# Kernel tuning notes

Measured on AMD Instinct MI355X. Metric: run time of the kernel, lower is better.

Reference implementation:

```python
import jax, jax.numpy as jnp
import numpy as np


def log_g(x):
    # log of the 'continuous' g: g(x) = x + 0.5 for x>=0, sigmoid(x) otherwise
    return jnp.where(x >= 0, jnp.log(jax.nn.relu(x) + 0.5), -jax.nn.softplus(-x))


def setup_inputs() -> dict:
    key = jax.random.key(0)
    ks = jax.random.split(key, 6)
    B, T, D, H = 8, 4096, 1024, 1024
    s = 1.0 / np.sqrt(D)
    return {
        "x": jax.random.normal(ks[0], (B, T, D), dtype=jnp.float32),
        "h_0": jax.random.uniform(ks[1], (B, 1, H), dtype=jnp.float32),
        "Wz": jax.random.normal(ks[2], (D, H), dtype=jnp.float32) * s,
        "bz": jnp.zeros((H,), dtype=jnp.float32),
        "Wh": jax.random.normal(ks[3], (D, H), dtype=jnp.float32) * s,
        "bh": jnp.zeros((H,), dtype=jnp.float32),
    }


def reference(x, h_0, Wz, bz, Wh, bh):
    # x: [B,T,D], h_0: [B,1,H]
    k = jnp.einsum('btd,dh->bth', x, Wz) + bz            # gate pre-activation
    log_z = -jax.nn.softplus(-k)                          # log sigmoid(k)
    log_coeffs = -jax.nn.softplus(k)                      # log (1 - sigmoid(k))
    log_h0 = log_g(h_0)                                   # [B,1,H]
    log_tilde_h = log_g(jnp.einsum('btd,dh->bth', x, Wh) + bh)
    # parallel scan in log space over time axis
    a_star = jnp.pad(jnp.cumsum(log_coeffs, axis=1), ((0, 0), (1, 0), (0, 0)))  # [B,T+1,H]
    log_values = jnp.concatenate([log_h0, log_z + log_tilde_h], axis=1)          # [B,T+1,H]
    log_h = a_star + jax.lax.cumlogsumexp(log_values - a_star, axis=1)
    return jnp.exp(log_h)  # [B,T+1,H]
```

## Files before the change

kernel.cpp:

```cpp
#include <hip/hip_runtime.h>
#include <hip/hip_bf16.h>
#include <cstdint>
#include <cstddef>

#define B_ 8
#define T_ 4096
#define D_ 1024
#define H_ 1024
#define M_ (B_*T_)
#define NCHUNK 64
#define CLEN 64

using bf16x8   = __attribute__((ext_vector_type(8))) __bf16;
using floatx4  = __attribute__((ext_vector_type(4))) float;
using float4v  = __attribute__((ext_vector_type(4))) float;
using ushort4v = __attribute__((ext_vector_type(4))) unsigned short;
using aw2_t    = __attribute__((ext_vector_type(2))) _Float16;
using halfx8   = __attribute__((ext_vector_type(8))) _Float16;

__device__ inline unsigned short f2bf(float f) {
  union { float f; unsigned u; } v; v.f = f;
  unsigned u = v.u;
  u += 0x7fffu + ((u >> 16) & 1u);
  return (unsigned short)(u >> 16);
}

__device__ inline void async_load16(const void* g, void* l) {
  __builtin_amdgcn_global_load_lds((const __attribute__((address_space(1))) void*)g,
                                   (__attribute__((address_space(3))) void*)l,
                                   16, 0, 0);
}

__global__ __launch_bounds__(256) void cast_x_kernel(const float* __restrict__ x,
                                                     unsigned short* __restrict__ xb) {
  size_t i = ((size_t)blockIdx.x * 256 + threadIdx.x) * 2;
#pragma unroll
  for (int j = 0; j < 2; ++j) {
    float4v v = ((const float4v*)x)[i + j];
    ushort4v o = { f2bf(v[0]), f2bf(v[1]), f2bf(v[2]), f2bf(v[3]) };
    ((ushort4v*)xb)[i + j] = o;
  }
}

__global__ __launch_bounds__(256) void transpose_w_kernel(const float* __restrict__ Wz,
                                                          const float* __restrict__ Wh,
                                                          unsigned short* __restrict__ Wzt,
                                                          unsigned short* __restrict__ Wht) {
  __shared__ float tile[32][33];
  const float* W = blockIdx.z ? Wh : Wz;
  unsigned short* Wt = blockIdx.z ? Wht : Wzt;
  int n0 = blockIdx.x * 32, k0 = blockIdx.y * 32;
#pragma unroll
  for (int j = 0; j < 4; ++j) {
    int kr = threadIdx.y + j * 8;
    tile[kr][threadIdx.x] = W[(size_t)(k0 + kr) * H_ + n0 + threadIdx.x];
  }
  __syncthreads();
#pragma unroll
  for (int j = 0; j < 4; ++j) {
    int nr = threadIdx.y + j * 8;
    Wt[(size_t)(n0 + nr) * D_ + k0 + threadIdx.x] = f2bf(tile[threadIdx.x][nr]);
  }
}

__global__ __launch_bounds__(256, 2) void gemm_kernel(
    const unsigned short* __restrict__ xb,
    const unsigned short* __restrict__ wzt,
    const unsigned short* __restrict__ wht,
    const float* __restrict__ bz, const float* __restrict__ bh,
    aw2_t* __restrict__ aw_out) {
  __shared__ __align__(16) unsigned short ldsA[128 * 32];
  __shared__ __align__(16) unsigned short ldsBz[128 * 32];
  __shared__ __align__(16) unsigned short ldsBh[128 * 32];

  const int tid = threadIdx.x;
  const int lane = tid & 63, wid = tid >> 6;
  const int wm = wid >> 1, wn = wid & 1;
  const int row16 = lane & 15, quad = lane >> 4;

  int g = blockIdx.x;
  int x = g & 7, j = g >> 3;
  int n_idx = j & 7;
  int m_idx = (x << 5) | (j >> 3);
  const int m0 = m_idx * 128, n0 = n_idx * 128;

  floatx4 accz[4][4], acch[4][4];
#pragma unroll
  for (int mi = 0; mi < 4; ++mi)
#pragma unroll
    for (int ni = 0; ni < 4; ++ni) {
      accz[mi][ni] = (floatx4){0.f, 0.f, 0.f, 0.f};
      acch[mi][ni] = (floatx4){0.f, 0.f, 0.f, 0.f};
    }

  const unsigned short* a0 = xb  + (size_t)(m0 + (tid >> 2)) * D_ + (tid & 3) * 8;
  const unsigned short* a1 = xb  + (size_t)(m0 + 64 + (tid >> 2)) * D_ + (tid & 3) * 8;
  const unsigned short* z0 = wzt + (size_t)(n0 + (tid >> 2)) * D_ + (tid & 3) * 8;
  const unsigned short* z1 = wzt + (size_t)(n0 + 64 + (tid >> 2)) * D_ + (tid & 3) * 8;
  const unsigned short* h0p = wht + (size_t)(n0 + (tid >> 2)) * D_ + (tid & 3) * 8;
  const unsigned short* h1p = wht + (size_t)(n0 + 64 + (tid >> 2)) * D_ + (tid & 3) * 8;

  for (int kk = 0; kk < D_; kk += 32) {
    async_load16(a0 + kk, &ldsA[tid * 8]);
    async_load16(a1 + kk, &ldsA[(tid + 256) * 8]);
    async_load16(z0 + kk, &ldsBz[tid * 8]);
    async_load16(z1 + kk, &ldsBz[(tid + 256) * 8]);
    async_load16(h0p + kk, &ldsBh[tid * 8]);
    async_load16(h1p + kk, &ldsBh[(tid + 256) * 8]);
    __syncthreads();

    bf16x8 af[4], bzf[4], bhf[4];
#pragma unroll
    for (int mi = 0; mi < 4; ++mi)
      af[mi] = *(const bf16x8*)&ldsA[(wm * 64 + mi * 16 + row16) * 32 + quad * 8];
#pragma unroll
    for (int ni = 0; ni < 4; ++ni) {
      bzf[ni] = *(const bf16x8*)&ldsBz[(wn * 64 + ni * 16 + row16) * 32 + quad * 8];
      bhf[ni] = *(const bf16x8*)&ldsBh[(wn * 64 + ni * 16 + row16) * 32 + quad * 8];
    }
#pragma unroll
    for (int mi = 0; mi < 4; ++mi)
#pragma unroll
      for (int ni = 0; ni < 4; ++ni) {
        accz[mi][ni] = __builtin_amdgcn_mfma_f32_16x16x32_bf16(af[mi], bzf[ni], accz[mi][ni], 0, 0, 0);
        acch[mi][ni] = __builtin_amdgcn_mfma_f32_16x16x32_bf16(af[mi], bhf[ni], acch[mi][ni], 0, 0, 0);
      }
    __syncthreads();
  }

#pragma unroll
  for (int mi = 0; mi < 4; ++mi) {
#pragma unroll
    for (int ni = 0; ni < 4; ++ni) {
      int col = n0 + wn * 64 + ni * 16 + row16;
      float bzv = bz[col], bhv = bh[col];
#pragma unroll
      for (int r = 0; r < 4; ++r) {
        int row = m0 + wm * 64 + mi * 16 + quad * 4 + r;
        float k   = accz[mi][ni][r] + bzv;
        float pre = acch[mi][ni][r] + bhv;
        float z  = 1.f / (1.f + __expf(-k));
        float av = 1.f / (1.f + __expf(k));
        float gg = (pre >= 0.f) ? (pre + 0.5f) : 1.f / (1.f + __expf(-pre));
        aw2_t o = { (_Float16)av, (_Float16)(z * gg) };
        aw_out[(size_t)row * H_ + col] = o;
      }
    }
  }
}

__global__ __launch_bounds__(256) void scan_pass1(const halfx8* __restrict__ aw,
                                                  float* __restrict__ P, float* __restrict__ S) {
  int c = blockIdx.x;
  int b = blockIdx.y;
  int h4 = threadIdx.x;
  size_t base = (size_t)(b * T_ + c * CLEN) * (H_ / 4) + h4;
  float p0 = 1.f, p1 = 1.f, p2 = 1.f, p3 = 1.f;
  float s0 = 0.f, s1 = 0.f, s2 = 0.f, s3 = 0.f;
#pragma unroll 8
  for (int i = 0; i < CLEN; ++i) {
    halfx8 v = aw[base + (size_t)i * (H_ / 4)];
    float a0 = (float)v[0], w0 = (float)v[1];
    float a1 = (float)v[2], w1 = (float)v[3];
    float a2 = (float)v[4], w2 = (float)v[5];
    float a3 = (float)v[6], w3 = (float)v[7];
    s0 = a0 * s0 + w0; p0 *= a0;
    s1 = a1 * s1 + w1; p1 *= a1;
    s2 = a2 * s2 + w2; p2 *= a2;
    s3 = a3 * s3 + w3; p3 *= a3;
  }
  size_t o = ((size_t)b * H_ + h4 * 4) * NCHUNK + c;
  P[o] = p0; P[o + NCHUNK] = p1; P[o + 2 * NCHUNK] = p2; P[o + 3 * NCHUNK] = p3;
  S[o] = s0; S[o + NCHUNK] = s1; S[o + 2 * NCHUNK] = s2; S[o + 3 * NCHUNK] = s3;
}

__global__ __launch_bounds__(256) void scan_pass2(const float* __restrict__ h0,
                                                  const float* __restrict__ P,
                                                  const float* __restrict__ S,
                                                  float* __restrict__ carry,
                                                  float* __restrict__ out) {
  int gid = blockIdx.x * 256 + threadIdx.x;
  int b = gid >> 10, h = gid & 1023;
  float v = h0[(size_t)b * H_ + h];
  float cur = (v >= 0.f) ? (v + 0.5f) : 1.f / (1.f + __expf(-v));
  out[((size_t)b * (T_ + 1)) * H_ + h] = cur;
  const float4v* Pv = (const float4v*)&P[((size_t)b * H_ + h) * NCHUNK];
  const float4v* Sv = (const float4v*)&S[((size_t)b * H_ + h) * NCHUNK];
  float4v* Cv = (float4v*)&carry[((size_t)b * H_ + h) * NCHUNK];
#pragma unroll
  for (int j = 0; j < NCHUNK / 4; ++j) {
    float4v p = Pv[j], s = Sv[j], cc;
    cc[0] = cur; cur = p[0] * cur + s[0];
    cc[1] = cur; cur = p[1] * cur + s[1];
    cc[2] = cur; cur = p[2] * cur + s[2];
    cc[3] = cur; cur = p[3] * cur + s[3];
    Cv[j] = cc;
  }
}

__global__ __launch_bounds__(256) void scan_pass3(const halfx8* __restrict__ aw,
                                                  const float* __restrict__ carry,
                                                  float* __restrict__ out) {
  int c = blockIdx.x;
  int b = blockIdx.y;
  int h4 = threadIdx.x;
  size_t base = (size_t)(b * T_ + c * CLEN) * (H_ / 4) + h4;
  size_t cb = ((size_t)b * H_ + h4 * 4) * NCHUNK + c;
  float c0 = carry[cb], c1 = carry[cb + NCHUNK], c2 = carry[cb + 2 * NCHUNK], c3 = carry[cb + 3 * NCHUNK];
  size_t obase = ((size_t)b * (T_ + 1) + c * CLEN + 1) * (H_ / 4) + h4;
  float4v* outv = (float4v*)out;
#pragma unroll 8
  for (int i = 0; i < CLEN; ++i) {
    halfx8 v = aw[base + (size_t)i * (H_ / 4)];
    c0 = (float)v[0] * c0 + (float)v[1];
    c1 = (float)v[2] * c1 + (float)v[3];
    c2 = (float)v[4] * c2 + (float)v[5];
    c3 = (float)v[6] * c3 + (float)v[7];
    float4v o = { c0, c1, c2, c3 };
    outv[obase + (size_t)i * (H_ / 4)] = o;
  }
}

extern "C" void kernel_launch(void* const* d_in, const int* in_sizes, int n_in,
                              void* d_out, int out_size, void* d_ws, size_t ws_size,
                              hipStream_t stream) {
  const float* x  = (const float*)d_in[0];
  const float* h0 = (const float*)d_in[1];
  const float* Wz = (const float*)d_in[2];
  const float* bz = (const float*)d_in[3];
  const float* Wh = (const float*)d_in[4];
  const float* bh = (const float*)d_in[5];
  float* out = (float*)d_out;

  char* ws = (char*)d_ws;
  unsigned short* xb  = (unsigned short*)(ws);
  unsigned short* wzt = (unsigned short*)(ws + 67108864ULL);
  unsigned short* wht = (unsigned short*)(ws + 69206016ULL);
  aw2_t* aw_ws = (aw2_t*)(ws + 71303168ULL);
  float* P_ws  = (float*)(ws + 71303168ULL + 134217728ULL);
  float* S_ws  = (float*)(ws + 71303168ULL + 134217728ULL + 2097152ULL);
  float* c_ws  = (float*)(ws + 71303168ULL + 134217728ULL + 2ULL * 2097152ULL);

  hipLaunchKernelGGL(cast_x_kernel, dim3(16384), dim3(256), 0, stream, x, xb);
  hipLaunchKernelGGL(transpose_w_kernel, dim3(32, 32, 2), dim3(32, 8), 0, stream, Wz, Wh, wzt, wht);
  hipLaunchKernelGGL(gemm_kernel, dim3(2048), dim3(256), 0, stream,
                     xb, wzt, wht, bz, bh, aw_ws);
  hipLaunchKernelGGL(scan_pass1, dim3(NCHUNK, B_), dim3(256), 0, stream,
                     (const halfx8*)aw_ws, P_ws, S_ws);
  hipLaunchKernelGGL(scan_pass2, dim3(32), dim3(256), 0, stream, h0, P_ws, S_ws, c_ws, out);
  hipLaunchKernelGGL(scan_pass3, dim3(NCHUNK, B_), dim3(256), 0, stream,
                     (const halfx8*)aw_ws, c_ws, out);
}
```

Measured before the change: 493.5 us.

## Double GEMM K-tile to 64 and swizzle LDS layout to avoid bank conflicts

The fused dual GEMM now stages a 64-wide K slice per iteration instead of 32, which halves the number of barrier pairs per tile. It also applies an XOR/rotation swizzle to the 16-byte chunks in LDS so that MFMA fragment reads spread across banks. The cost is doubled LDS use (48KB per block), which may limit occupancy at two blocks per CU.

```diff
diff --git a/kernel.cpp b/kernel.cpp
--- a/kernel.cpp
+++ b/kernel.cpp
@@ -69,9 +69,9 @@
     const unsigned short* __restrict__ wht,
     const float* __restrict__ bz, const float* __restrict__ bh,
     aw2_t* __restrict__ aw_out) {
-  __shared__ __align__(16) unsigned short ldsA[128 * 32];
-  __shared__ __align__(16) unsigned short ldsBz[128 * 32];
-  __shared__ __align__(16) unsigned short ldsBh[128 * 32];
+  __shared__ __align__(16) unsigned short ldsA[128 * 64];
+  __shared__ __align__(16) unsigned short ldsBz[128 * 64];
+  __shared__ __align__(16) unsigned short ldsBh[128 * 64];
 
   const int tid = threadIdx.x;
   const int lane = tid & 63, wid = tid >> 6;
@@ -93,38 +93,46 @@
       acch[mi][ni] = (floatx4){0.f, 0.f, 0.f, 0.f};
     }
 
-  const unsigned short* a0 = xb  + (size_t)(m0 + (tid >> 2)) * D_ + (tid & 3) * 8;
-  const unsigned short* a1 = xb  + (size_t)(m0 + 64 + (tid >> 2)) * D_ + (tid & 3) * 8;
-  const unsigned short* z0 = wzt + (size_t)(n0 + (tid >> 2)) * D_ + (tid & 3) * 8;
-  const unsigned short* z1 = wzt + (size_t)(n0 + 64 + (tid >> 2)) * D_ + (tid & 3) * 8;
-  const unsigned short* h0p = wht + (size_t)(n0 + (tid >> 2)) * D_ + (tid & 3) * 8;
-  const unsigned short* h1p = wht + (size_t)(n0 + 64 + (tid >> 2)) * D_ + (tid & 3) * 8;
-
-  for (int kk = 0; kk < D_; kk += 32) {
-    async_load16(a0 + kk, &ldsA[tid * 8]);
-    async_load16(a1 + kk, &ldsA[(tid + 256) * 8]);
-    async_load16(z0 + kk, &ldsBz[tid * 8]);
-    async_load16(z1 + kk, &ldsBz[(tid + 256) * 8]);
-    async_load16(h0p + kk, &ldsBh[tid * 8]);
-    async_load16(h1p + kk, &ldsBh[(tid + 256) * 8]);
+  const int srow = tid >> 3;
+  const int jblk = ((tid & 7) - srow) & 7;
+  const unsigned short* aSrc  = xb  + (size_t)(m0 + srow) * D_ + jblk * 8;
+  const unsigned short* zSrc  = wzt + (size_t)(n0 + srow) * D_ + jblk * 8;
+  const unsigned short* hSrc  = wht + (size_t)(n0 + srow) * D_ + jblk * 8;
+
+  const int p0 = (quad + row16) & 7;
+  const int p1 = p0 ^ 4;
+
+  for (int kk = 0; kk < D_; kk += 64) {
+#pragma unroll
+    for (int t = 0; t < 4; ++t) {
+      size_t roff = (size_t)(32 * t) * D_ + kk;
+      int doff = (tid + 256 * t) * 8;
+      async_load16(aSrc + roff, &ldsA[doff]);
+      async_load16(zSrc + roff, &ldsBz[doff]);
+      async_load16(hSrc + roff, &ldsBh[doff]);
+    }
     __syncthreads();
 
-    bf16x8 af[4], bzf[4], bhf[4];
-#pragma unroll
-    for (int mi = 0; mi < 4; ++mi)
-      af[mi] = *(const bf16x8*)&ldsA[(wm * 64 + mi * 16 + row16) * 32 + quad * 8];
-#pragma unroll
-    for (int ni = 0; ni < 4; ++ni) {
-      bzf[ni] = *(const bf16x8*)&ldsBz[(wn * 64 + ni * 16 + row16) * 32 + quad * 8];
-      bhf[ni] = *(const bf16x8*)&ldsBh[(wn * 64 + ni * 16 + row16) * 32 + quad * 8];
-    }
-#pragma unroll
-    for (int mi = 0; mi < 4; ++mi)
+#pragma unroll
+    for (int kh = 0; kh < 2; ++kh) {
+      const int p = kh ? p1 : p0;
+      bf16x8 af[4], bzf[4], bhf[4];
+#pragma unroll
+      for (int mi = 0; mi < 4; ++mi)
+        af[mi] = *(const bf16x8*)&ldsA[(wm * 64 + mi * 16 + row16) * 64 + p * 8];
 #pragma unroll
       for (int ni = 0; ni < 4; ++ni) {
-        accz[mi][ni] = __builtin_amdgcn_mfma_f32_16x16x32_bf16(af[mi], bzf[ni], accz[mi][ni], 0, 0, 0);
-        acch[mi][ni] = __builtin_amdgcn_mfma_f32_16x16x32_bf16(af[mi], bhf[ni], acch[mi][ni], 0, 0, 0);
+        bzf[ni] = *(const bf16x8*)&ldsBz[(wn * 64 + ni * 16 + row16) * 64 + p * 8];
+        bhf[ni] = *(const bf16x8*)&ldsBh[(wn * 64 + ni * 16 + row16) * 64 + p * 8];
       }
+#pragma unroll
+      for (int mi = 0; mi < 4; ++mi)
+#pragma unroll
+        for (int ni = 0; ni < 4; ++ni) {
+          accz[mi][ni] = __builtin_amdgcn_mfma_f32_16x16x32_bf16(af[mi], bzf[ni], accz[mi][ni], 0, 0, 0);
+          acch[mi][ni] = __builtin_amdgcn_mfma_f32_16x16x32_bf16(af[mi], bhf[ni], acch[mi][ni], 0, 0, 0);
+        }
+    }
     __syncthreads();
   }
 
```

New measurement: 472.8 us. -4.2%, faster.
